# Optimization experiments

Hardware: AMD Instinct MI355X
Metric: run time of the kernel (lower is better)

The kernel has to match this reference:

```python
import jax, jax.numpy as jnp
import numpy as np

NUM_TILES = 64
TPC = 8            # tiles per cluster
GRID = 16          # spline grid size
EPS = 1e-5


def setup_inputs() -> dict:
    key = jax.random.key(0)
    ks = jax.random.split(key, 6)
    B, S, D, T, DH, G = 2, 1024, 512, NUM_TILES, 128, GRID
    x = jax.random.normal(ks[0], (B, S, D), dtype=jnp.float32)
    gamma = jnp.ones((D,), jnp.float32)
    beta = jnp.zeros((D,), jnp.float32)
    # torch layouts: down.weight [DH, D], up.weight [D, DH]
    Wd = jax.random.normal(ks[1], (T, DH, D), dtype=jnp.float32) * 0.02
    spline_bases = jax.random.normal(ks[2], (T, DH, G), dtype=jnp.float32) * 0.1
    spline_slopes = jax.random.normal(ks[3], (T, DH, G), dtype=jnp.float32) * 0.1
    Wu = jax.random.normal(ks[4], (T, D, DH), dtype=jnp.float32) * 0.02
    scale = jnp.full((T,), 0.1, jnp.float32)
    return {"x": x, "gamma": gamma, "beta": beta, "Wd": Wd,
            "spline_bases": spline_bases, "spline_slopes": spline_slopes,
            "Wu": Wu, "scale": scale}


def reference(x, gamma, beta, Wd, spline_bases, spline_slopes, Wu, scale):
    B, S, D = x.shape
    T, DH, _ = Wd.shape
    C = T // TPC
    N = B * S

    # LayerNorm
    mu = x.mean(-1, keepdims=True)
    var = ((x - mu) ** 2).mean(-1, keepdims=True)
    xn = (x - mu) * jax.lax.rsqrt(var + EPS) * gamma + beta
    xf = xn.reshape(N, D)

    # Signatures (first call: ema == current tile signatures)
    tile_sigs = jnp.sign(Wd.mean(axis=1))                         # [T, D]
    cluster_sigs = jnp.sign(tile_sigs.reshape(C, TPC, D).mean(1))  # [C, D]

    # Hierarchical routing: cluster -> tile
    in_sigs = jnp.sign(xf)                                        # [N, D]
    best_c = jnp.argmax(in_sigs @ cluster_sigs.T, axis=-1)        # [N]
    tile_scores = (in_sigs @ tile_sigs.T).reshape(N, C, TPC)      # [N, C, TPC]
    sc = jnp.take_along_axis(tile_scores, best_c[:, None, None], axis=1)[:, 0, :]
    local_best = jnp.argmax(sc, axis=-1)                          # [N]
    tidx = best_c * TPC + local_best                              # [N]

    # Dispatch: gather per-token expert weights, down-project
    h = jnp.einsum('nd,nhd->nh', xf, Wd[tidx])                    # [N, DH]

    # Spline nonlinearity
    hn = jax.nn.sigmoid(h)
    idx = jnp.clip((hn * GRID).astype(jnp.int32), 0, GRID - 1)    # [N, DH]
    base = jnp.take_along_axis(spline_bases[tidx], idx[..., None], axis=-1)[..., 0]
    slope = jnp.take_along_axis(spline_slopes[tidx], idx[..., None], axis=-1)[..., 0]
    local_pos = hn * GRID - idx.astype(h.dtype)                   # (hn - idx*cell)/cell
    hs = base + slope * local_pos                                 # [N, DH]

    # Up-project, per-tile scale, combine (dropout is identity in eval)
    y = jnp.einsum('nh,ndh->nd', hs, Wu[tidx]) * scale[tidx][:, None]
    return x + y.reshape(B, S, D)
```

## Files before the change

kernel.cpp:

```cpp
#include <hip/hip_runtime.h>
#include <hip/hip_bf16.h>
#include <math.h>

#define NTILES 64
#define TPC 8
#define NCLUST 8
#define GRID_SZ 16
#define DIM 512
#define DHID 128
#define NTOK 2048
#define LN_EPS 1e-5f
#define TB 16
#define NCHUNK_MAX 192

typedef __attribute__((ext_vector_type(8))) short bf16x8;
typedef __attribute__((ext_vector_type(4))) unsigned short u16x4;
typedef __attribute__((ext_vector_type(4))) float f32x4;
typedef unsigned long long u64;

static __device__ __forceinline__ unsigned short bf16bits(float f) {
    union { __hip_bfloat16 h; unsigned short s; } u;
    u.h = __float2bfloat16(f);
    return u.s;
}

static __device__ __forceinline__ bf16x8 cvt8(const float* p) {
    float4 a = *(const float4*)p;
    float4 b = *(const float4*)(p + 4);
    float e[8] = {a.x, a.y, a.z, a.w, b.x, b.y, b.z, b.w};
    bf16x8 v;
    #pragma unroll
    for (int i = 0; i < 8; ++i) v[i] = (short)bf16bits(e[i]);
    return v;
}

static __device__ __forceinline__ u64 maj3(u64 a, u64 b, u64 c) {
    return (a & b) | (c & (a ^ b));
}

static __device__ __forceinline__ bool route_chunk(const int* counts, int lane, int cb,
                                                   int& t, int& base, int& m) {
    int cnt_l = counts[lane];
    int nck = (cnt_l + TB - 1) / TB;
    int pre = nck;
    #pragma unroll
    for (int off = 1; off < 64; off <<= 1) {
        int u = __shfl_up(pre, off);
        if (lane >= off) pre += u;
    }
    int total = __shfl(pre, 63);
    pre -= nck;
    if (cb >= total) return false;
    u64 msk = __ballot(cb >= pre && cb < pre + nck);
    t = (int)__builtin_ctzll(msk);
    base = (cb - __shfl(pre, t)) * TB;
    m = min(TB, __shfl(cnt_l, t) - base);
    return true;
}

__global__ __launch_bounds__(512) void k_prep(const float* __restrict__ x,
                                              const float* __restrict__ gamma,
                                              const float* __restrict__ beta,
                                              const float* __restrict__ Wd,
                                              const float* __restrict__ Wu,
                                              unsigned short* __restrict__ wd_b,
                                              unsigned short* __restrict__ wu_b,
                                              unsigned short* __restrict__ xn_b,
                                              u64* __restrict__ tbits,
                                              u64* __restrict__ xbits,
                                              int* __restrict__ counts) {
    int bid = blockIdx.x;
    int tid = threadIdx.x;
    int lane = tid & 63;
    int wv = tid >> 6;
    if (bid < NTILES) {
        int t = bid;
        if (bid == 0 && tid < NTILES) counts[tid] = 0;
        int q = tid >> 7;
        int c4 = tid & 127;
        const float* wp = Wd + ((size_t)t * DHID + q * 32) * DIM + c4 * 4;
        unsigned short* bp = wd_b + ((size_t)t * DHID + q * 32) * DIM + c4 * 4;
        float4 a = {0.f, 0.f, 0.f, 0.f};
        #pragma unroll
        for (int jb = 0; jb < 4; ++jb) {
            float4 v[8];
            #pragma unroll
            for (int u = 0; u < 8; ++u)
                v[u] = *(const float4*)(wp + (size_t)(jb * 8 + u) * DIM);
            #pragma unroll
            for (int u = 0; u < 8; ++u) {
                u16x4 h = {bf16bits(v[u].x), bf16bits(v[u].y), bf16bits(v[u].z), bf16bits(v[u].w)};
                *(u16x4*)(bp + (size_t)(jb * 8 + u) * DIM) = h;
                a.x += v[u].x; a.y += v[u].y; a.z += v[u].z; a.w += v[u].w;
            }
        }
        __shared__ float ps[4][DIM];
        *(float4*)&ps[q][c4 * 4] = a;
        __syncthreads();
        float s = ps[0][tid] + ps[1][tid] + ps[2][tid] + ps[3][tid];
        u64 b = __ballot(s < 0.f);
        if (lane == 0) tbits[t * 8 + wv] = b;
    } else if (bid < 320) {
        int n = (bid - NTILES) * 8 + wv;
        const float* xr = x + (size_t)n * DIM;
        float v[8];
        float sum = 0.f;
        #pragma unroll
        for (int j = 0; j < 8; ++j) { float t = xr[lane + 64 * j]; v[j] = t; sum += t; }
        #pragma unroll
        for (int off = 32; off; off >>= 1) sum += __shfl_xor(sum, off);
        float mu = sum * (1.f / DIM);
        float sq = 0.f;
        #pragma unroll
        for (int j = 0; j < 8; ++j) { float t = v[j] - mu; sq += t * t; }
        #pragma unroll
        for (int off = 32; off; off >>= 1) sq += __shfl_xor(sq, off);
        float rs = rsqrtf(sq * (1.f / DIM) + LN_EPS);
        #pragma unroll
        for (int j = 0; j < 8; ++j) {
            int d = lane + 64 * j;
            float xv = (v[j] - mu) * rs * gamma[d] + beta[d];
            unsigned short us = bf16bits(xv);
            xn_b[(size_t)n * DIM + d] = us;
            u64 bb = __ballot((us & 0x8000u) != 0 && (us & 0x7fffu) != 0);
            if (lane == 0) xbits[n * 8 + j] = bb;
        }
    } else {
        size_t basei = (size_t)(bid - 320) * 16384;
        #pragma unroll
        for (int k = 0; k < 4; ++k) {
            size_t off = basei + (size_t)tid * 8 + (size_t)k * 4096;
            *(bf16x8*)(wu_b + off) = cvt8(Wu + off);
        }
    }
}

__global__ __launch_bounds__(256) void k_route(const u64* __restrict__ xbits,
                                               const u64* __restrict__ tbits,
                                               int* __restrict__ counts,
                                               int* __restrict__ list) {
    int n = blockIdx.x * 4 + (threadIdx.x >> 6);
    int lane = threadIdx.x & 63;
    u64 xb[8];
    #pragma unroll
    for (int j = 0; j < 8; ++j) xb[j] = xbits[n * 8 + j];
    const u64* tb = tbits + lane * 8;
    int ts = 0;
    #pragma unroll
    for (int j = 0; j < 8; ++j) ts += __popcll(xb[j] ^ tb[j]);
    int tscore = DIM - 2 * ts;

    int c = lane >> 3, jw = lane & 7;
    u64 x0 = tbits[(c * TPC + 0) * 8 + jw], x1 = tbits[(c * TPC + 1) * 8 + jw];
    u64 x2 = tbits[(c * TPC + 2) * 8 + jw], x3 = tbits[(c * TPC + 3) * 8 + jw];
    u64 x4 = tbits[(c * TPC + 4) * 8 + jw], x5 = tbits[(c * TPC + 5) * 8 + jw];
    u64 x6 = tbits[(c * TPC + 6) * 8 + jw], x7 = tbits[(c * TPC + 7) * 8 + jw];
    u64 s0 = x0 ^ x1 ^ x2, c0 = maj3(x0, x1, x2);
    u64 s1 = x3 ^ x4 ^ x5, c1 = maj3(x3, x4, x5);
    u64 s2 = x6 ^ x7,      c2 = x6 & x7;
    u64 t0 = s0 ^ s1 ^ s2, t1 = maj3(s0, s1, s2);
    u64 p = c0 ^ c1, q = c0 & c1;
    u64 r = c2 ^ t1, s_ = c2 & t1;
    u64 S0 = p ^ r, car = p & r;
    u64 W0 = (q ^ s_) ^ car;
    u64 W1 = (q & s_) | (car & (q ^ s_));
    u64 cbit = W1 | (W0 & (S0 | t0));
    u64 cmsk = ~(W0 & ~W1 & ~S0 & ~t0);
    int psc = __popcll(cmsk) - 2 * __popcll((xb[jw] ^ cbit) & cmsk);
    psc += __shfl_xor(psc, 1);
    psc += __shfl_xor(psc, 2);
    psc += __shfl_xor(psc, 4);

    int bc = 0, best = __shfl(psc, 0);
    #pragma unroll
    for (int k = 1; k < NCLUST; ++k) {
        int v = __shfl(psc, k * 8);
        if (v > best) { best = v; bc = k; }
    }
    int bt = bc * TPC, bts = __shfl(tscore, bc * TPC);
    #pragma unroll
    for (int k = 1; k < TPC; ++k) {
        int v = __shfl(tscore, bc * TPC + k);
        if (v > bts) { bts = v; bt = bc * TPC + k; }
    }
    if (lane == 0) {
        int slot = atomicAdd(&counts[bt], 1);
        list[(size_t)bt * NTOK + slot] = n;
    }
}

__global__ __launch_bounds__(512, 1) void k_ffn(const float* __restrict__ x,
                                                const unsigned short* __restrict__ xn_b,
                                                const unsigned short* __restrict__ wd_b,
                                                const float* __restrict__ sb,
                                                const float* __restrict__ ss,
                                                const unsigned short* __restrict__ wu_b,
                                                const float* __restrict__ scale,
                                                const int* __restrict__ counts,
                                                const int* __restrict__ list,
                                                float* __restrict__ out) {
    int tid = threadIdx.x;
    int lane = tid & 63;
    int wv = tid >> 6;
    int cb = ((int)blockIdx.x & 7) * (NCHUNK_MAX / 8) + ((int)blockIdx.x >> 3);
    int t, base, m;
    if (!route_chunk(counts, lane, cb, t, base, m)) return;

    __shared__ __align__(16) unsigned short hsl[TB * DHID];

    int mrow = lane & 15;
    int ko = (lane >> 4) * 8;
    int tokm = list[(size_t)t * NTOK + base + min(mrow, m - 1)];

    const unsigned short* xr = xn_b + (size_t)tokm * DIM;
    const unsigned short* wr = wd_b + ((size_t)t * DHID + wv * 16 + mrow) * DIM;
    bf16x8 wreg[16], areg[16];
    #pragma unroll
    for (int kk = 0; kk < 16; ++kk) {
        int d = kk * 32 + ko;
        wreg[kk] = *(const bf16x8*)(wr + d);
        areg[kk] = *(const bf16x8*)(xr + d);
    }
    f32x4 acc0 = {0.f, 0.f, 0.f, 0.f}, acc1 = acc0;
    #pragma unroll
    for (int kk = 0; kk < 8; ++kk) {
        acc0 = __builtin_amdgcn_mfma_f32_16x16x32_bf16(areg[2 * kk], wreg[2 * kk], acc0, 0, 0, 0);
        acc1 = __builtin_amdgcn_mfma_f32_16x16x32_bf16(areg[2 * kk + 1], wreg[2 * kk + 1], acc1, 0, 0, 0);
    }
    f32x4 acc = acc0 + acc1;

    bf16x8 wupf[16];
    #pragma unroll
    for (int nt = 0; nt < 4; ++nt) {
        const unsigned short* wru = wu_b + ((size_t)t * DIM + wv * 64 + nt * 16 + mrow) * DHID;
        #pragma unroll
        for (int kk = 0; kk < 4; ++kk)
            wupf[nt * 4 + kk] = *(const bf16x8*)(wru + kk * 32 + ko);
    }

    int dh = wv * 16 + mrow;
    const float* sbt = sb + ((size_t)t * DHID + dh) * GRID_SZ;
    const float* sst = ss + ((size_t)t * DHID + dh) * GRID_SZ;
    #pragma unroll
    for (int r = 0; r < 4; ++r) {
        int tr = (lane >> 4) * 4 + r;
        float h = acc[r];
        float hn = 1.f / (1.f + expf(-h));
        float g = hn * (float)GRID_SZ;
        int idx = (int)g;
        idx = idx > GRID_SZ - 1 ? GRID_SZ - 1 : idx;
        float lp = g - (float)idx;
        float val = sbt[idx] + sst[idx] * lp;
        hsl[(tr * DHID + dh) ^ ((tr & 7) << 3)] = bf16bits(val);
    }
    __syncthreads();

    float sc_t = scale[t];
    bf16x8 a2[4];
    #pragma unroll
    for (int kk = 0; kk < 4; ++kk)
        a2[kk] = *(const bf16x8*)&hsl[(mrow * DHID + kk * 32 + ko) ^ ((mrow & 7) << 3)];
    #pragma unroll
    for (int nt = 0; nt < 4; ++nt) {
        int d = wv * 64 + nt * 16 + mrow;
        f32x4 au = {0.f, 0.f, 0.f, 0.f};
        #pragma unroll
        for (int kk = 0; kk < 4; ++kk)
            au = __builtin_amdgcn_mfma_f32_16x16x32_bf16(a2[kk], wupf[nt * 4 + kk], au, 0, 0, 0);
        #pragma unroll
        for (int r = 0; r < 4; ++r) {
            int tr = (lane >> 4) * 4 + r;
            int tok_tr = __shfl(tokm, tr);
            if (tr < m) {
                size_t o = (size_t)tok_tr * DIM + d;
                out[o] = x[o] + au[r] * sc_t;
            }
        }
    }
}

extern "C" void kernel_launch(void* const* d_in, const int* in_sizes, int n_in,
                              void* d_out, int out_size, void* d_ws, size_t ws_size,
                              hipStream_t stream) {
    const float* x     = (const float*)d_in[0];
    const float* gamma = (const float*)d_in[1];
    const float* beta  = (const float*)d_in[2];
    const float* Wd    = (const float*)d_in[3];
    const float* sb    = (const float*)d_in[4];
    const float* ss    = (const float*)d_in[5];
    const float* Wu    = (const float*)d_in[6];
    const float* scale = (const float*)d_in[7];
    float* out = (float*)d_out;

    u64*   tbits         = (u64*)d_ws;
    u64*   xbits         = tbits + NTILES * 8;
    int*   counts        = (int*)(xbits + (size_t)NTOK * 8);
    int*   list          = counts + NTILES;
    unsigned short* xn_b = (unsigned short*)(list + (size_t)NTILES * NTOK);
    unsigned short* wd_b = xn_b + (size_t)NTOK * DIM;
    unsigned short* wu_b = wd_b + (size_t)NTILES * DHID * DIM;

    k_prep<<<576, 512, 0, stream>>>(x, gamma, beta, Wd, Wu, wd_b, wu_b, xn_b, tbits, xbits, counts);
    k_route<<<NTOK / 4, 256, 0, stream>>>(xbits, tbits, counts, list);
    k_ffn<<<NCHUNK_MAX, 512, 0, stream>>>(x, xn_b, wd_b, sb, ss, wu_b, scale, counts, list, out);
}
```

Baseline: 46.27 us.

## Split Wd conversion into separate wider kernel and use nontemporal stores

Moves the Wd fp32-to-bf16 conversion and column-sum into a new kernel that runs 256 blocks (four per tile) instead of 64. Each block writes partial column sums to a workspace buffer, and k_prep reduces those partials into tile sign bits. Stores of the bf16 copies, xn and xbits now use nontemporal stores. This should cut the long per-block serial loop over 128 rows that limited the prep phase, at the cost of one more kernel launch and an extra round trip for the partial sums.

After: 50.40 us. 8.9% more time.

```diff
diff --git a/kernel.cpp b/kernel.cpp
--- a/kernel.cpp
+++ b/kernel.cpp
@@ -58,50 +58,60 @@
     return true;
 }
 
+__global__ __launch_bounds__(512) void k_psum(const float* __restrict__ Wd,
+                                              unsigned short* __restrict__ wd_b,
+                                              float* __restrict__ psum,
+                                              int* __restrict__ counts) {
+    int bid = blockIdx.x;
+    int t = bid >> 2, q = bid & 3;
+    int tid = threadIdx.x;
+    if (bid == 0 && tid < NTILES) counts[tid] = 0;
+    int r0 = tid >> 7;
+    int c4 = tid & 127;
+    const float* wp = Wd + ((size_t)t * DHID + q * 32 + r0 * 8) * DIM + c4 * 4;
+    unsigned short* bp = wd_b + ((size_t)t * DHID + q * 32 + r0 * 8) * DIM + c4 * 4;
+    float4 v[8];
+    #pragma unroll
+    for (int k = 0; k < 8; ++k) v[k] = *(const float4*)(wp + (size_t)k * DIM);
+    float4 a = {0.f, 0.f, 0.f, 0.f};
+    #pragma unroll
+    for (int k = 0; k < 8; ++k) {
+        u16x4 h = {bf16bits(v[k].x), bf16bits(v[k].y), bf16bits(v[k].z), bf16bits(v[k].w)};
+        __builtin_nontemporal_store(h, (u16x4*)(bp + (size_t)k * DIM));
+        a.x += v[k].x; a.y += v[k].y; a.z += v[k].z; a.w += v[k].w;
+    }
+    __shared__ float ps[4][DIM];
+    *(float4*)&ps[r0][c4 * 4] = a;
+    __syncthreads();
+    float s = ps[0][tid] + ps[1][tid] + ps[2][tid] + ps[3][tid];
+    __builtin_nontemporal_store(s, &psum[(size_t)(t * 4 + q) * DIM + tid]);
+}
+
 __global__ __launch_bounds__(512) void k_prep(const float* __restrict__ x,
                                               const float* __restrict__ gamma,
                                               const float* __restrict__ beta,
-                                              const float* __restrict__ Wd,
                                               const float* __restrict__ Wu,
-                                              unsigned short* __restrict__ wd_b,
+                                              const float* __restrict__ psum,
                                               unsigned short* __restrict__ wu_b,
                                               unsigned short* __restrict__ xn_b,
                                               u64* __restrict__ tbits,
-                                              u64* __restrict__ xbits,
-                                              int* __restrict__ counts) {
+                                              u64* __restrict__ xbits) {
     int bid = blockIdx.x;
     int tid = threadIdx.x;
     int lane = tid & 63;
     int wv = tid >> 6;
-    if (bid < NTILES) {
-        int t = bid;
-        if (bid == 0 && tid < NTILES) counts[tid] = 0;
-        int q = tid >> 7;
-        int c4 = tid & 127;
-        const float* wp = Wd + ((size_t)t * DHID + q * 32) * DIM + c4 * 4;
-        unsigned short* bp = wd_b + ((size_t)t * DHID + q * 32) * DIM + c4 * 4;
-        float4 a = {0.f, 0.f, 0.f, 0.f};
-        #pragma unroll
-        for (int jb = 0; jb < 4; ++jb) {
-            float4 v[8];
-            #pragma unroll
-            for (int u = 0; u < 8; ++u)
-                v[u] = *(const float4*)(wp + (size_t)(jb * 8 + u) * DIM);
-            #pragma unroll
-            for (int u = 0; u < 8; ++u) {
-                u16x4 h = {bf16bits(v[u].x), bf16bits(v[u].y), bf16bits(v[u].z), bf16bits(v[u].w)};
-                *(u16x4*)(bp + (size_t)(jb * 8 + u) * DIM) = h;
-                a.x += v[u].x; a.y += v[u].y; a.z += v[u].z; a.w += v[u].w;
-            }
+    if (bid < 8) {
+        int t = bid * 8 + wv;
+        #pragma unroll
+        for (int jw = 0; jw < 8; ++jw) {
+            int d = jw * 64 + lane;
+            float s = psum[(size_t)(t * 4 + 0) * DIM + d] + psum[(size_t)(t * 4 + 1) * DIM + d]
+                    + psum[(size_t)(t * 4 + 2) * DIM + d] + psum[(size_t)(t * 4 + 3) * DIM + d];
+            u64 b = __ballot(s < 0.f);
+            if (lane == 0) tbits[t * 8 + jw] = b;
         }
-        __shared__ float ps[4][DIM];
-        *(float4*)&ps[q][c4 * 4] = a;
-        __syncthreads();
-        float s = ps[0][tid] + ps[1][tid] + ps[2][tid] + ps[3][tid];
-        u64 b = __ballot(s < 0.f);
-        if (lane == 0) tbits[t * 8 + wv] = b;
-    } else if (bid < 320) {
-        int n = (bid - NTILES) * 8 + wv;
+    } else if (bid < 264) {
+        int n = (bid - 8) * 8 + wv;
         const float* xr = x + (size_t)n * DIM;
         float v[8];
         float sum = 0.f;
@@ -121,16 +131,16 @@
             int d = lane + 64 * j;
             float xv = (v[j] - mu) * rs * gamma[d] + beta[d];
             unsigned short us = bf16bits(xv);
-            xn_b[(size_t)n * DIM + d] = us;
+            __builtin_nontemporal_store(us, &xn_b[(size_t)n * DIM + d]);
             u64 bb = __ballot((us & 0x8000u) != 0 && (us & 0x7fffu) != 0);
-            if (lane == 0) xbits[n * 8 + j] = bb;
+            if (lane == 0) __builtin_nontemporal_store(bb, &xbits[n * 8 + j]);
         }
     } else {
-        size_t basei = (size_t)(bid - 320) * 16384;
+        size_t basei = (size_t)(bid - 264) * 16384;
         #pragma unroll
         for (int k = 0; k < 4; ++k) {
             size_t off = basei + (size_t)tid * 8 + (size_t)k * 4096;
-            *(bf16x8*)(wu_b + off) = cvt8(Wu + off);
+            __builtin_nontemporal_store(cvt8(Wu + off), (bf16x8*)(wu_b + off));
         }
     }
 }
@@ -296,11 +306,13 @@
     u64*   xbits         = tbits + NTILES * 8;
     int*   counts        = (int*)(xbits + (size_t)NTOK * 8);
     int*   list          = counts + NTILES;
-    unsigned short* xn_b = (unsigned short*)(list + (size_t)NTILES * NTOK);
+    float* psum          = (float*)(list + (size_t)NTILES * NTOK);
+    unsigned short* xn_b = (unsigned short*)(psum + 256 * DIM);
     unsigned short* wd_b = xn_b + (size_t)NTOK * DIM;
     unsigned short* wu_b = wd_b + (size_t)NTILES * DHID * DIM;
 
-    k_prep<<<576, 512, 0, stream>>>(x, gamma, beta, Wd, Wu, wd_b, wu_b, xn_b, tbits, xbits, counts);
+    k_psum<<<256, 512, 0, stream>>>(Wd, wd_b, psum, counts);
+    k_prep<<<520, 512, 0, stream>>>(x, gamma, beta, Wu, psum, wu_b, xn_b, tbits, xbits);
     k_route<<<NTOK / 4, 256, 0, stream>>>(xbits, tbits, counts, list);
     k_ffn<<<NCHUNK_MAX, 512, 0, stream>>>(x, xn_b, wd_b, sb, ss, wu_b, scale, counts, list, out);
 }
```
